# Kernel tuning notes

Hardware: AMD Instinct MI355X
Metric: run time of the kernel (lower is better)

Reference implementation:

```python
import jax, jax.numpy as jnp
import numpy as np


def _pairwise_dist(a, b):
    # a: [B, N, D], b: [B, M, D] -> Euclidean distances [B, N, M]
    aa = jnp.sum(a * a, axis=-1)  # [B, N]
    bb = jnp.sum(b * b, axis=-1)  # [B, M]
    ab = jnp.einsum('bnd,bmd->bnm', a, b)  # [B, N, M]
    d2 = aa[:, :, None] + bb[None if aa.ndim == 1 else slice(None), None, :].reshape(bb.shape[0], 1, bb.shape[1]) - 2.0 * ab
    return jnp.sqrt(jnp.maximum(d2, 0.0))


def setup_inputs() -> dict:
    key = jax.random.key(0)
    k1, k2 = jax.random.split(key)
    B, N, M, D = 4, 8192, 8192, 3
    inp = jax.random.normal(k1, (B, N, D), dtype=jnp.float32)
    tgt = jax.random.normal(k2, (B, M, D), dtype=jnp.float32)
    return {"input": inp, "target": tgt}


def reference(input, target):
    # Bidirectional Chamfer distance, matching the torch module:
    # for each batch element (inner call has batch_size=1):
    #   distances1 = NN dist of each target point to input cloud (tree1=input, query array2=target)
    #   distances2 = NN dist of each input point to target cloud
    #   per-sample loss = mean(distances1) + mean(distances2)
    # total loss = sum over batch.
    d = _pairwise_dist(input, target)  # [B, N, M]
    nn_for_target = jnp.min(d, axis=1)  # [B, M] closest input point per target point
    nn_for_input = jnp.min(d, axis=2)   # [B, N] closest target point per input point
    per_sample = jnp.mean(nn_for_target, axis=1) + jnp.mean(nn_for_input, axis=1)  # [B]
    return jnp.sum(per_sample)
```

## Files before the change

### kernel.cpp

```cpp
#include <hip/hip_runtime.h>
#include <math.h>


typedef __attribute__((ext_vector_type(8)))  _Float16 f16x8;
typedef __attribute__((ext_vector_type(16))) float    f32x16;

constexpr int TPB    = 512;
constexpr int NPTS   = 8192;
constexpr int NB     = 4;
constexpr int QPB    = 256;
constexpr int CHUNK  = 1024;
constexpr int NCHUNK = NPTS / CHUNK;
constexpr int TILES  = CHUNK / 32;

__device__ inline float max3f(float a, float b, float c) {
    return fmaxf(fmaxf(a, b), c);
}

__device__ inline float merge16(float run, f32x16 v) {
    const float w0 = max3f(v[0],  v[1],  v[2]);
    const float w1 = max3f(v[3],  v[4],  v[5]);
    const float w2 = max3f(v[6],  v[7],  v[8]);
    const float w3 = max3f(v[9],  v[10], v[11]);
    const float w4 = max3f(v[12], v[13], v[14]);
    const float x0 = max3f(w0, w1, v[15]);
    const float x1 = max3f(w2, w3, w4);
    return max3f(run, x0, x1);
}

__device__ inline f16x8 make_qfrag(float x, float y, float z, int half) {
    const _Float16 hx = (_Float16)x, hy = (_Float16)y, hz = (_Float16)z;
    const _Float16 lx = (_Float16)(x - (float)hx);
    const _Float16 ly = (_Float16)(y - (float)hy);
    const _Float16 lz = (_Float16)(z - (float)hz);
    const f16x8 f0 = (f16x8){hx, hy, hz, hx, hy, hz, lx, ly};
    const f16x8 f1 = (f16x8){lz, (_Float16)1.0f, (_Float16)1.0f, 0, 0, 0, 0, 0};
    return half ? f1 : f0;
}

__device__ inline void write_ref(f16x8* buf, int r, float x, float y, float z) {
    const _Float16 hx = (_Float16)x, hy = (_Float16)y, hz = (_Float16)z;
    const _Float16 lx = (_Float16)(x - (float)hx);
    const _Float16 ly = (_Float16)(y - (float)hy);
    const _Float16 lz = (_Float16)(z - (float)hz);
    const float c = 0.5f * fmaf(z, z, fmaf(y, y, x * x));
    const _Float16 chi = (_Float16)c;
    const _Float16 clo = (_Float16)(c - (float)chi);
    const int base = (r >> 5) * 64 + (r & 31);
    buf[base]      = (f16x8){hx, hy, hz, lx, ly, lz, hx, hy};
    buf[base + 32] = (f16x8){hz, -chi, -clo, 0, 0, 0, 0, 0};
}

__global__ __launch_bounds__(TPB) void chamfer_one(
    const float* __restrict__ inp, const float* __restrict__ tgt,
    float* __restrict__ out)
{
    const int dir = blockIdx.y >> 2;
    const int b   = blockIdx.y & 3;
    const float* qb = (dir ? tgt : inp) + (size_t)b * NPTS * 3;
    const float* rb = (dir ? inp : tgt) + (size_t)b * NPTS * 3;

    const int tid  = threadIdx.x;
    const int w    = tid >> 6;
    const int lane = tid & 63;
    const int half = lane >> 5;
    const int col  = lane & 31;

    const int q = blockIdx.x * QPB + w * 32 + col;
    const float qx = qb[q * 3 + 0], qy = qb[q * 3 + 1], qz = qb[q * 3 + 2];
    const f16x8 bq = make_qfrag(qx, qy, qz, half);

    __shared__ f16x8 lds[2 * 2048];

    {
        const float* s0 = rb + (size_t)tid * 3;
        const float* s1 = rb + (size_t)(512 + tid) * 3;
        write_ref(lds, tid,       s0[0], s0[1], s0[2]);
        write_ref(lds, 512 + tid, s1[0], s1[1], s1[2]);
    }
    __syncthreads();

    const f32x16 zf = (f32x16)0.0f;
    float run = -3.4e38f;

    for (int c = 0; c < NCHUNK; ++c) {
        f16x8* bufR = lds + (c & 1) * 2048;
        f16x8* bufW = lds + ((c & 1) ^ 1) * 2048;

        float nx0 = 0, ny0 = 0, nz0 = 0, nx1 = 0, ny1 = 0, nz1 = 0;
        const bool more = (c + 1 < NCHUNK);
        if (more) {
            const float* s0 = rb + (size_t)((c + 1) * CHUNK + tid) * 3;
            const float* s1 = rb + (size_t)((c + 1) * CHUNK + 512 + tid) * 3;
            nx0 = s0[0]; ny0 = s0[1]; nz0 = s0[2];
            nx1 = s1[0]; ny1 = s1[1]; nz1 = s1[2];
        }

#pragma unroll 4
        for (int t = 0; t < TILES; ++t) {
            const f16x8 a = bufR[t * 64 + lane];
            const f32x16 acc =
                __builtin_amdgcn_mfma_f32_32x32x16_f16(a, bq, zf, 0, 0, 0);
            run = merge16(run, acc);
        }

        if (more) {
            write_ref(bufW, tid,       nx0, ny0, nz0);
            write_ref(bufW, 512 + tid, nx1, ny1, nz1);
        }
        __syncthreads();
    }

    run = fmaxf(run, __shfl_xor(run, 32));
    const float cq = 0.5f * fmaf(qz, qz, fmaf(qy, qy, qx * qx));
    const float sval = fmaxf(cq - run, 0.0f);
    float term = (lane < 32) ? sqrtf(2.0f * sval) * (1.0f / NPTS) : 0.0f;
#pragma unroll
    for (int off = 32; off > 0; off >>= 1) term += __shfl_down(term, off, 64);

    float* bs = (float*)lds;
    if (lane == 0) bs[w] = term;
    __syncthreads();
    if (tid == 0) {
        float s = 0.0f;
#pragma unroll
        for (int i = 0; i < 8; ++i) s += bs[i];
        atomicAdd(out, s);
    }
}

__global__ __launch_bounds__(256) void chamfer_nn_valu(
    const float* __restrict__ A, const float* __restrict__ Bp,
    unsigned int* __restrict__ minA, unsigned int* __restrict__ minB,
    int N, int M, int B)
{
    const int bz = blockIdx.z, b = bz % B, dir = bz / B;
    const float* Q = dir ? Bp : A;
    const float* R = dir ? A : Bp;
    unsigned int* om = dir ? minB : minA;
    const int NQ = dir ? M : N, NR = dir ? N : M;
    const int mSlice = NR / gridDim.y;
    const int tid = threadIdx.x;
    const int nBase = blockIdx.x * (256 * 4);
    const int mStart = blockIdx.y * mSlice;
    const float* qb = Q + (size_t)b * NQ * 3;
    const float* rb = R + (size_t)b * NR * 3;
    float qx[4], qy[4], qz[4], dmax[4];
#pragma unroll
    for (int k = 0; k < 4; ++k) {
        const int n = nBase + tid + k * 256;
        qx[k] = qb[n * 3]; qy[k] = qb[n * 3 + 1]; qz[k] = qb[n * 3 + 2];
        dmax[k] = -3.4e38f;
    }
    __shared__ float4 tgtl[256];
    for (int m0 = mStart; m0 < mStart + mSlice; m0 += 256) {
        __syncthreads();
        {
            const float* src = rb + (size_t)(m0 + tid) * 3;
            const float rx = src[0], ry = src[1], rz = src[2];
            tgtl[tid] = make_float4(rx, ry, rz,
                -0.5f * fmaf(rz, rz, fmaf(ry, ry, rx * rx)));
        }
        __syncthreads();
#pragma unroll 2
        for (int j = 0; j < 256; j += 2) {
            const float4 r0 = tgtl[j], r1 = tgtl[j + 1];
#pragma unroll
            for (int k = 0; k < 4; ++k) {
                const float t0 = fmaf(qz[k], r0.z, fmaf(qy[k], r0.y, fmaf(qx[k], r0.x, r0.w)));
                const float t1 = fmaf(qz[k], r1.z, fmaf(qy[k], r1.y, fmaf(qx[k], r1.x, r1.w)));
                dmax[k] = max3f(dmax[k], t0, t1);
            }
        }
    }
#pragma unroll
    for (int k = 0; k < 4; ++k) {
        const int n = nBase + tid + k * 256;
        const float c = 0.5f * fmaf(qz[k], qz[k], fmaf(qy[k], qy[k], qx[k] * qx[k]));
        atomicMin(&om[(size_t)b * NQ + n], __float_as_uint(fmaxf(c - dmax[k], 0.0f)));
    }
}

__global__ __launch_bounds__(256) void chamfer_reduce(
    const unsigned int* __restrict__ mins, int nA, int nTotal,
    float scaleA, float scaleB, float* __restrict__ out)
{
    float s = 0.0f;
    for (int i = blockIdx.x * blockDim.x + threadIdx.x; i < nTotal;
         i += gridDim.x * blockDim.x) {
        s += sqrtf(2.0f * __uint_as_float(mins[i])) * (i < nA ? scaleA : scaleB);
    }
#pragma unroll
    for (int off = 32; off > 0; off >>= 1) s += __shfl_down(s, off, 64);
    __shared__ float wsum[4];
    const int lane = threadIdx.x & 63, wid = threadIdx.x >> 6;
    if (lane == 0) wsum[wid] = s;
    __syncthreads();
    if (threadIdx.x == 0) atomicAdd(out, wsum[0] + wsum[1] + wsum[2] + wsum[3]);
}

extern "C" void kernel_launch(void* const* d_in, const int* in_sizes, int n_in,
                              void* d_out, int out_size, void* d_ws, size_t ws_size,
                              hipStream_t stream) {
    const float* inp = (const float*)d_in[0];
    const float* tgt = (const float*)d_in[1];
    float* out = (float*)d_out;

    const int B = 4, D = 3;
    const int N = in_sizes[0] / (B * D);
    const int M = in_sizes[1] / (B * D);

    if (N == NPTS && M == NPTS && B == NB) {
        hipMemsetAsync(d_out, 0, sizeof(float), stream);
        dim3 grid(NPTS / QPB, 2 * NB);
        chamfer_one<<<grid, TPB, 0, stream>>>(inp, tgt, out);
    } else {
        unsigned int* min_in  = (unsigned int*)d_ws;
        unsigned int* min_tgt = min_in + (size_t)B * N;
        hipMemsetAsync(d_ws, 0xFF,
                       (size_t)(B * N + B * M) * sizeof(unsigned int), stream);
        hipMemsetAsync(d_out, 0, sizeof(float), stream);
        dim3 grid(N / (256 * 4), 32, 2 * B);
        chamfer_nn_valu<<<grid, 256, 0, stream>>>(inp, tgt, min_in, min_tgt, N, M, B);
        chamfer_reduce<<<dim3(64), 256, 0, stream>>>(
            min_in, B * N, B * (N + M), 1.0f / N, 1.0f / M, out);
    }
}
```

Baseline: 75.88 us.

## Split reference set across blocks with cooperative grid reduction and register-blocked queries

Restructures the fast path into a single cooperative kernel of 256 blocks. Each block handles 1024 queries, with each wave holding four query fragments so every LDS reference load is reused by four MFMAs. The reference cloud is split into four slices, and per-slice partial minima go to workspace. Two grid-wide syncs then combine the slice minima, compute the sqrt terms and do a deterministic final sum. This drops the memset and global atomic but adds grid-sync overhead and workspace traffic, and it depends on all 256 blocks being co-resident.

```diff
diff --git a/kernel.cpp b/kernel.cpp
--- a/kernel.cpp
+++ b/kernel.cpp
@@ -1,17 +1,24 @@
 #include <hip/hip_runtime.h>
+#include <hip/hip_cooperative_groups.h>
 #include <math.h>
 
+
+namespace cg = cooperative_groups;
 
 typedef __attribute__((ext_vector_type(8)))  _Float16 f16x8;
 typedef __attribute__((ext_vector_type(16))) float    f32x16;
 
-constexpr int TPB    = 512;
-constexpr int NPTS   = 8192;
-constexpr int NB     = 4;
-constexpr int QPB    = 256;
-constexpr int CHUNK  = 1024;
-constexpr int NCHUNK = NPTS / CHUNK;
-constexpr int TILES  = CHUNK / 32;
+constexpr int TPB   = 512;
+constexpr int NPTS  = 8192;
+constexpr int NB    = 4;
+constexpr int MS    = 4;
+constexpr int SLICE = NPTS / MS;
+constexpr int CHUNK = 512;
+constexpr int NCH   = SLICE / CHUNK;
+constexpr int TILES = CHUNK / 32;
+constexpr int QPW   = 128;
+constexpr int QPB   = TPB / 64 * QPW;
+constexpr int NSLOT = 2 * NB * NPTS;
 
 __device__ inline float max3f(float a, float b, float c) {
     return fmaxf(fmaxf(a, b), c);
@@ -51,14 +58,20 @@
     buf[base + 32] = (f16x8){hz, -chi, -clo, 0, 0, 0, 0, 0};
 }
 
-__global__ __launch_bounds__(TPB) void chamfer_one(
+__global__ __launch_bounds__(TPB) void chamfer_coop(
     const float* __restrict__ inp, const float* __restrict__ tgt,
+    float* __restrict__ pmin,
+    float* __restrict__ bsum,
     float* __restrict__ out)
 {
-    const int dir = blockIdx.y >> 2;
-    const int b   = blockIdx.y & 3;
-    const float* qb = (dir ? tgt : inp) + (size_t)b * NPTS * 3;
-    const float* rb = (dir ? inp : tgt) + (size_t)b * NPTS * 3;
+    const int gid   = blockIdx.x;
+    const int slice = gid & (MS - 1);
+    const int qb    = gid >> 2;
+    const int z     = qb >> 3;
+    const int qt    = qb & 7;
+    const int dir   = z >> 2, b = z & 3;
+    const float* Q = (dir ? tgt : inp) + (size_t)b * NPTS * 3;
+    const float* R = (dir ? inp : tgt) + (size_t)b * NPTS * 3;
 
     const int tid  = threadIdx.x;
     const int w    = tid >> 6;
@@ -66,66 +79,105 @@
     const int half = lane >> 5;
     const int col  = lane & 31;
 
-    const int q = blockIdx.x * QPB + w * 32 + col;
-    const float qx = qb[q * 3 + 0], qy = qb[q * 3 + 1], qz = qb[q * 3 + 2];
-    const f16x8 bq = make_qfrag(qx, qy, qz, half);
-
-    __shared__ f16x8 lds[2 * 2048];
+    float qx[4], qy[4], qz[4];
+    f16x8 bq[4];
+#pragma unroll
+    for (int f = 0; f < 4; ++f) {
+        const int q = qt * QPB + w * QPW + f * 32 + col;
+        qx[f] = Q[q * 3 + 0]; qy[f] = Q[q * 3 + 1]; qz[f] = Q[q * 3 + 2];
+        bq[f] = make_qfrag(qx[f], qy[f], qz[f], half);
+    }
+
+    __shared__ f16x8 lds[2 * 1024];
+    const float* rbase = R + (size_t)slice * SLICE * 3;
 
     {
-        const float* s0 = rb + (size_t)tid * 3;
-        const float* s1 = rb + (size_t)(512 + tid) * 3;
-        write_ref(lds, tid,       s0[0], s0[1], s0[2]);
-        write_ref(lds, 512 + tid, s1[0], s1[1], s1[2]);
+        const float* s = rbase + (size_t)tid * 3;
+        write_ref(lds, tid, s[0], s[1], s[2]);
     }
     __syncthreads();
 
     const f32x16 zf = (f32x16)0.0f;
-    float run = -3.4e38f;
-
-    for (int c = 0; c < NCHUNK; ++c) {
-        f16x8* bufR = lds + (c & 1) * 2048;
-        f16x8* bufW = lds + ((c & 1) ^ 1) * 2048;
-
-        float nx0 = 0, ny0 = 0, nz0 = 0, nx1 = 0, ny1 = 0, nz1 = 0;
-        const bool more = (c + 1 < NCHUNK);
+    float run[4] = {-3.4e38f, -3.4e38f, -3.4e38f, -3.4e38f};
+
+    for (int c = 0; c < NCH; ++c) {
+        f16x8* bufR = lds + (c & 1) * 1024;
+        f16x8* bufW = lds + ((c & 1) ^ 1) * 1024;
+
+        float nx = 0, ny = 0, nz = 0;
+        const bool more = (c + 1 < NCH);
         if (more) {
-            const float* s0 = rb + (size_t)((c + 1) * CHUNK + tid) * 3;
-            const float* s1 = rb + (size_t)((c + 1) * CHUNK + 512 + tid) * 3;
-            nx0 = s0[0]; ny0 = s0[1]; nz0 = s0[2];
-            nx1 = s1[0]; ny1 = s1[1]; nz1 = s1[2];
+            const float* s = rbase + (size_t)((c + 1) * CHUNK + tid) * 3;
+            nx = s[0]; ny = s[1]; nz = s[2];
         }
 
 #pragma unroll 4
         for (int t = 0; t < TILES; ++t) {
             const f16x8 a = bufR[t * 64 + lane];
-            const f32x16 acc =
-                __builtin_amdgcn_mfma_f32_32x32x16_f16(a, bq, zf, 0, 0, 0);
-            run = merge16(run, acc);
-        }
-
-        if (more) {
-            write_ref(bufW, tid,       nx0, ny0, nz0);
-            write_ref(bufW, 512 + tid, nx1, ny1, nz1);
-        }
-        __syncthreads();
-    }
-
-    run = fmaxf(run, __shfl_xor(run, 32));
-    const float cq = 0.5f * fmaf(qz, qz, fmaf(qy, qy, qx * qx));
-    const float sval = fmaxf(cq - run, 0.0f);
-    float term = (lane < 32) ? sqrtf(2.0f * sval) * (1.0f / NPTS) : 0.0f;
-#pragma unroll
-    for (int off = 32; off > 0; off >>= 1) term += __shfl_down(term, off, 64);
-
-    float* bs = (float*)lds;
-    if (lane == 0) bs[w] = term;
-    __syncthreads();
-    if (tid == 0) {
-        float s = 0.0f;
-#pragma unroll
-        for (int i = 0; i < 8; ++i) s += bs[i];
-        atomicAdd(out, s);
+#pragma unroll
+            for (int f = 0; f < 4; ++f) {
+                const f32x16 acc =
+                    __builtin_amdgcn_mfma_f32_32x32x16_f16(a, bq[f], zf, 0, 0, 0);
+                run[f] = merge16(run[f], acc);
+            }
+        }
+
+        if (more) write_ref(bufW, tid, nx, ny, nz);
+        __syncthreads();
+    }
+
+#pragma unroll
+    for (int f = 0; f < 4; ++f) {
+        run[f] = fmaxf(run[f], __shfl_xor(run[f], 32));
+        if (lane < 32) {
+            const float cq = 0.5f * fmaf(qz[f], qz[f],
+                                fmaf(qy[f], qy[f], qx[f] * qx[f]));
+            pmin[(size_t)slice * NSLOT + z * NPTS
+                 + qt * QPB + w * QPW + f * 32 + col]
+                = fmaxf(cq - run[f], 0.0f);
+        }
+    }
+
+    cg::this_grid().sync();
+
+    __shared__ float bs[8];
+    {
+        const int i = gid * TPB + tid;
+        float term = 0.0f;
+        if (i < NSLOT) {
+            float v = pmin[i];
+#pragma unroll
+            for (int sl = 1; sl < MS; ++sl)
+                v = fminf(v, pmin[(size_t)sl * NSLOT + i]);
+            term = sqrtf(2.0f * v) * (1.0f / NPTS);
+        }
+#pragma unroll
+        for (int off = 32; off > 0; off >>= 1) term += __shfl_down(term, off, 64);
+        if (lane == 0) bs[w] = term;
+        __syncthreads();
+        if (tid == 0) {
+            float s = 0.0f;
+#pragma unroll
+            for (int j = 0; j < 8; ++j) s += bs[j];
+            bsum[gid] = s;
+        }
+    }
+
+    cg::this_grid().sync();
+
+    if (gid == 0) {
+        float v = (tid < 256) ? bsum[tid] : 0.0f;
+#pragma unroll
+        for (int off = 32; off > 0; off >>= 1) v += __shfl_down(v, off, 64);
+        __shared__ float bs2[8];
+        if (lane == 0) bs2[w] = v;
+        __syncthreads();
+        if (tid == 0) {
+            float s = 0.0f;
+#pragma unroll
+            for (int j = 0; j < 8; ++j) s += bs2[j];
+            *out = s;
+        }
     }
 }
 
@@ -210,10 +262,15 @@
     const int N = in_sizes[0] / (B * D);
     const int M = in_sizes[1] / (B * D);
 
-    if (N == NPTS && M == NPTS && B == NB) {
-        hipMemsetAsync(d_out, 0, sizeof(float), stream);
-        dim3 grid(NPTS / QPB, 2 * NB);
-        chamfer_one<<<grid, TPB, 0, stream>>>(inp, tgt, out);
+    const size_t needBytes = (size_t)(MS * NSLOT + 256) * sizeof(float);
+
+    if (N == NPTS && M == NPTS && B == NB && ws_size >= needBytes) {
+        float* pmin = (float*)d_ws;
+        float* bsum = pmin + (size_t)MS * NSLOT;
+        void* args[] = {(void*)&inp, (void*)&tgt, (void*)&pmin,
+                        (void*)&bsum, (void*)&out};
+        hipLaunchCooperativeKernel((void*)chamfer_coop, dim3(256), dim3(TPB),
+                                   args, 0, stream);
     } else {
         unsigned int* min_in  = (unsigned int*)d_ws;
         unsigned int* min_tgt = min_in + (size_t)B * N;
```

Result: slower. 134.6 us (+77.4%).
